# Optimization experiments

Hardware: AMD Instinct MI355X
Metric: run time of the kernel (lower is better)

The kernel has to match this reference:

```python
import jax, jax.numpy as jnp
import numpy as np


def setup_inputs() -> dict:
    key = jax.random.key(0)
    x = jax.random.normal(key, (8192, 16384), dtype=jnp.float32)
    return {"x": x, "k": 64}


def reference(x, k):
    # top-k values along last dim (sorted descending); threshold = k-th largest
    vals = jax.lax.top_k(x, k)[0]            # [B, k]
    thresh = vals[..., -1:]                   # min of top-k == last sorted value
    return jnp.where(x >= thresh, x, jnp.zeros_like(x))
```

## Files before the change

### kernel.cpp

```cpp
#include <hip/hip_runtime.h>
#include <stdint.h>

#define COLS 16384
#define TPB 1024
#define NWAVES 16
#define EPT 16
#define F4PT 4
#define ROUNDS 16

__device__ __forceinline__ unsigned f2k(unsigned u) {
    return (u & 0x80000000u) ? ~u : (u | 0x80000000u);
}

__device__ __forceinline__ unsigned sbcnt(unsigned long long m) {
    unsigned c;
    asm("s_bcnt1_i32_b64 %0, %1" : "=s"(c) : "s"(m) : "scc");
    return c;
}

__global__ __launch_bounds__(TPB, 8) void topk_row_kernel(
        const float* __restrict__ x,
        const int* __restrict__ kptr,
        float* __restrict__ out) {
    const int tid  = threadIdx.x;
    const int wid  = tid >> 6;
    const int lane = tid & 63;
    const size_t base = (size_t)blockIdx.x * (size_t)COLS;
    const float4* __restrict__ xin  = (const float4*)(x + base);
    float4*       __restrict__ xout = (float4*)(out + base);

    const int k = __builtin_amdgcn_readfirstlane(kptr[0]);

    __shared__ unsigned long long slot[ROUNDS * NWAVES];

    float4 v[F4PT];
    unsigned key[EPT];
#pragma unroll
    for (int i = 0; i < F4PT; ++i) {
        v[i] = xin[i * TPB + tid];
        key[i*4+0] = f2k(__float_as_uint(v[i].x));
        key[i*4+1] = f2k(__float_as_uint(v[i].y));
        key[i*4+2] = f2k(__float_as_uint(v[i].z));
        key[i*4+3] = f2k(__float_as_uint(v[i].w));
    }

    uint64_t lo = 0, hi = 1ull << 32;
#pragma unroll 1
    for (int r = 0; r < ROUNDS; ++r) {
        const uint64_t w  = hi - lo;
        const uint64_t q1 = lo + (w >> 2);
        const uint64_t q2 = lo + (w >> 1);
        const uint64_t q3 = q1 + (w >> 1);
        const unsigned t1 = (unsigned)q1;
        const unsigned t2 = (unsigned)q2;
        const unsigned t3 = (unsigned)q3;

        unsigned c1 = 0, c2 = 0, c3 = 0;
#pragma unroll
        for (int e = 0; e < EPT; ++e) {
            c1 += sbcnt(__builtin_amdgcn_ballot_w64(key[e] >= t1));
            c2 += sbcnt(__builtin_amdgcn_ballot_w64(key[e] >= t2));
            c3 += sbcnt(__builtin_amdgcn_ballot_w64(key[e] >= t3));
        }
        if (lane == 0)
            slot[r * NWAVES + wid] =
                (unsigned long long)c1 |
                ((unsigned long long)c2 << 21) |
                ((unsigned long long)c3 << 42);
        __syncthreads();

        unsigned long long s = slot[r * NWAVES + (lane & (NWAVES - 1))];
        s += __shfl_xor(s, 1);
        s += __shfl_xor(s, 2);
        s += __shfl_xor(s, 4);
        s += __shfl_xor(s, 8);
        const int cc1 = __builtin_amdgcn_readfirstlane((int)(s & 0x1FFFFFull));
        const int cc2 = __builtin_amdgcn_readfirstlane((int)((s >> 21) & 0x1FFFFFull));
        const int cc3 = __builtin_amdgcn_readfirstlane((int)(s >> 42));

        if (cc1 < k)      { hi = q1; }
        else if (cc2 < k) { lo = q1; hi = q2; }
        else if (cc3 < k) { lo = q2; hi = q3; }
        else              { lo = q3; }
    }

    const unsigned tk = (unsigned)lo;
#pragma unroll
    for (int i = 0; i < F4PT; ++i) {
        float4 o;
        o.x = (key[i*4+0] >= tk) ? v[i].x : 0.0f;
        o.y = (key[i*4+1] >= tk) ? v[i].y : 0.0f;
        o.z = (key[i*4+2] >= tk) ? v[i].z : 0.0f;
        o.w = (key[i*4+3] >= tk) ? v[i].w : 0.0f;
        xout[i * TPB + tid] = o;
    }
}

extern "C" void kernel_launch(void* const* d_in, const int* in_sizes, int n_in,
                              void* d_out, int out_size, void* d_ws, size_t ws_size,
                              hipStream_t stream) {
    const float* x  = (const float*)d_in[0];
    const int*   kp = (const int*)d_in[1];
    float*       o  = (float*)d_out;
    const int rows = in_sizes[0] / COLS;
    topk_row_kernel<<<rows, TPB, 0, stream>>>(x, kp, o);
}
```

Measured before the change: 1.184 ms.

## Replace block-wide quaternary search with per-wave top-k and candidate merge

Each wave now finds its own k-th largest key with a 32-step binary search that uses only ballots, with no block barriers. The block threshold is the max over waves. Keys above it, padded with ties, are compacted into shared memory as at most 16*k candidates. A second binary search over those candidates, held in registers, gives the exact k-th largest. Output values are rebuilt from the keys instead of keeping the original floats, which lowers register pressure. This removes 16 __syncthreads rounds, but assumes k <= 64 (KCAP) with no check, and the per-wave searches cost more ballot work.

```diff
diff --git a/kernel.cpp b/kernel.cpp
--- a/kernel.cpp
+++ b/kernel.cpp
@@ -6,16 +6,22 @@
 #define NWAVES 16
 #define EPT 16
 #define F4PT 4
-#define ROUNDS 16
+#define KCAP 64
 
 __device__ __forceinline__ unsigned f2k(unsigned u) {
     return (u & 0x80000000u) ? ~u : (u | 0x80000000u);
 }
-
+__device__ __forceinline__ unsigned k2f_bits(unsigned key) {
+    return (key & 0x80000000u) ? (key ^ 0x80000000u) : ~key;
+}
 __device__ __forceinline__ unsigned sbcnt(unsigned long long m) {
     unsigned c;
     asm("s_bcnt1_i32_b64 %0, %1" : "=s"(c) : "s"(m) : "scc");
     return c;
+}
+__device__ __forceinline__ unsigned rank_lt(unsigned long long m) {
+    unsigned r = __builtin_amdgcn_mbcnt_lo((unsigned)m, 0u);
+    return __builtin_amdgcn_mbcnt_hi((unsigned)(m >> 32), r);
 }
 
 __global__ __launch_bounds__(TPB, 8) void topk_row_kernel(
@@ -31,67 +37,96 @@
 
     const int k = __builtin_amdgcn_readfirstlane(kptr[0]);
 
-    __shared__ unsigned long long slot[ROUNDS * NWAVES];
+    __shared__ unsigned twv[NWAVES];
+    __shared__ unsigned cand[NWAVES * KCAP];
 
-    float4 v[F4PT];
     unsigned key[EPT];
 #pragma unroll
     for (int i = 0; i < F4PT; ++i) {
-        v[i] = xin[i * TPB + tid];
-        key[i*4+0] = f2k(__float_as_uint(v[i].x));
-        key[i*4+1] = f2k(__float_as_uint(v[i].y));
-        key[i*4+2] = f2k(__float_as_uint(v[i].z));
-        key[i*4+3] = f2k(__float_as_uint(v[i].w));
+        const float4 v = xin[i * TPB + tid];
+        key[i*4+0] = f2k(__float_as_uint(v.x));
+        key[i*4+1] = f2k(__float_as_uint(v.y));
+        key[i*4+2] = f2k(__float_as_uint(v.z));
+        key[i*4+3] = f2k(__float_as_uint(v.w));
     }
 
     uint64_t lo = 0, hi = 1ull << 32;
 #pragma unroll 1
-    for (int r = 0; r < ROUNDS; ++r) {
-        const uint64_t w  = hi - lo;
-        const uint64_t q1 = lo + (w >> 2);
-        const uint64_t q2 = lo + (w >> 1);
-        const uint64_t q3 = q1 + (w >> 1);
-        const unsigned t1 = (unsigned)q1;
-        const unsigned t2 = (unsigned)q2;
-        const unsigned t3 = (unsigned)q3;
+    for (int r = 0; r < 32; ++r) {
+        const uint64_t mid = lo + ((hi - lo) >> 1);
+        const unsigned t = (unsigned)mid;
+        unsigned c = 0;
+#pragma unroll
+        for (int e = 0; e < EPT; ++e)
+            c += sbcnt(__builtin_amdgcn_ballot_w64(key[e] >= t));
+        if ((int)c >= k) lo = mid; else hi = mid;
+    }
+    if (lane == 0) twv[wid] = (unsigned)lo;
+    __syncthreads();
 
-        unsigned c1 = 0, c2 = 0, c3 = 0;
+    unsigned tv = twv[lane & (NWAVES - 1)];
+    { unsigned o = __shfl_xor(tv, 1); tv = tv > o ? tv : o; }
+    { unsigned o = __shfl_xor(tv, 2); tv = tv > o ? tv : o; }
+    { unsigned o = __shfl_xor(tv, 4); tv = tv > o ? tv : o; }
+    { unsigned o = __shfl_xor(tv, 8); tv = tv > o ? tv : o; }
+    const unsigned tstar = (unsigned)__builtin_amdgcn_readfirstlane((int)tv);
+
+    const unsigned wbase = (unsigned)wid * (unsigned)k;
+    unsigned cb = 0;
 #pragma unroll
-        for (int e = 0; e < EPT; ++e) {
-            c1 += sbcnt(__builtin_amdgcn_ballot_w64(key[e] >= t1));
-            c2 += sbcnt(__builtin_amdgcn_ballot_w64(key[e] >= t2));
-            c3 += sbcnt(__builtin_amdgcn_ballot_w64(key[e] >= t3));
-        }
-        if (lane == 0)
-            slot[r * NWAVES + wid] =
-                (unsigned long long)c1 |
-                ((unsigned long long)c2 << 21) |
-                ((unsigned long long)c3 << 42);
-        __syncthreads();
+    for (int e = 0; e < EPT; ++e) {
+        const unsigned long long mb = __builtin_amdgcn_ballot_w64(key[e] > tstar);
+        if (key[e] > tstar) cand[wbase + cb + rank_lt(mb)] = key[e];
+        cb += sbcnt(mb);
+    }
+    unsigned meq = 0;
+#pragma unroll
+    for (int e = 0; e < EPT; ++e)
+        meq += sbcnt(__builtin_amdgcn_ballot_w64(key[e] == tstar));
+    for (unsigned j = (unsigned)lane; j < (unsigned)k; j += 64)
+        if (j >= cb) cand[wbase + j] = ((j - cb) < meq) ? tstar : 0u;
+    __syncthreads();
 
-        unsigned long long s = slot[r * NWAVES + (lane & (NWAVES - 1))];
-        s += __shfl_xor(s, 1);
-        s += __shfl_xor(s, 2);
-        s += __shfl_xor(s, 4);
-        s += __shfl_xor(s, 8);
-        const int cc1 = __builtin_amdgcn_readfirstlane((int)(s & 0x1FFFFFull));
-        const int cc2 = __builtin_amdgcn_readfirstlane((int)((s >> 21) & 0x1FFFFFull));
-        const int cc3 = __builtin_amdgcn_readfirstlane((int)(s >> 42));
+    const int total = NWAVES * k;
+    unsigned ck[16];
+#pragma unroll
+    for (int j = 0; j < 16; ++j) {
+        const int idx = j * 64 + lane;
+        ck[j] = (idx < total) ? cand[idx] : 0u;
+    }
+    unsigned wmax = 0;
+#pragma unroll
+    for (int j = 0; j < 16; ++j) wmax = wmax > ck[j] ? wmax : ck[j];
+    { unsigned o = __shfl_xor(wmax,  1); wmax = wmax > o ? wmax : o; }
+    { unsigned o = __shfl_xor(wmax,  2); wmax = wmax > o ? wmax : o; }
+    { unsigned o = __shfl_xor(wmax,  4); wmax = wmax > o ? wmax : o; }
+    { unsigned o = __shfl_xor(wmax,  8); wmax = wmax > o ? wmax : o; }
+    { unsigned o = __shfl_xor(wmax, 16); wmax = wmax > o ? wmax : o; }
+    { unsigned o = __shfl_xor(wmax, 32); wmax = wmax > o ? wmax : o; }
 
-        if (cc1 < k)      { hi = q1; }
-        else if (cc2 < k) { lo = q1; hi = q2; }
-        else if (cc3 < k) { lo = q2; hi = q3; }
-        else              { lo = q3; }
+    uint64_t lo2 = tstar;
+    uint64_t hi2 = (uint64_t)(unsigned)__builtin_amdgcn_readfirstlane((int)wmax) + 1;
+#pragma unroll 1
+    while (hi2 - lo2 > 1) {
+        const uint64_t mid = lo2 + ((hi2 - lo2) >> 1);
+        const unsigned t = (unsigned)mid;
+        unsigned c = 0;
+#pragma unroll
+        for (int j = 0; j < 16; ++j)
+            c += sbcnt(__builtin_amdgcn_ballot_w64(ck[j] >= t));
+        if ((int)c >= k) lo2 = mid; else hi2 = mid;
     }
 
-    const unsigned tk = (unsigned)lo;
+    const unsigned tk = (unsigned)lo2;
 #pragma unroll
     for (int i = 0; i < F4PT; ++i) {
         float4 o;
-        o.x = (key[i*4+0] >= tk) ? v[i].x : 0.0f;
-        o.y = (key[i*4+1] >= tk) ? v[i].y : 0.0f;
-        o.z = (key[i*4+2] >= tk) ? v[i].z : 0.0f;
-        o.w = (key[i*4+3] >= tk) ? v[i].w : 0.0f;
+        const unsigned k0 = key[i*4+0], k1 = key[i*4+1];
+        const unsigned k2 = key[i*4+2], k3 = key[i*4+3];
+        o.x = (k0 >= tk) ? __uint_as_float(k2f_bits(k0)) : 0.0f;
+        o.y = (k1 >= tk) ? __uint_as_float(k2f_bits(k1)) : 0.0f;
+        o.z = (k2 >= tk) ? __uint_as_float(k2f_bits(k2)) : 0.0f;
+        o.w = (k3 >= tk) ? __uint_as_float(k2f_bits(k3)) : 0.0f;
         xout[i * TPB + tid] = o;
     }
 }
```

After: 1.200 ms. Within noise of the previous version (+1.3%).
